# Kernel optimization log

Hardware: AMD Instinct MI355X
Metric: run time of the kernel (lower is better)

## Reference

```python
import jax, jax.numpy as jnp
import numpy as np

IN_F = 4096
OUT_F = 4096
RANK = 16
NUM_SLOTS = 32
ALPHA = 1.0


def setup_inputs() -> dict:
    key = jax.random.key(0)
    k_x, k_w, k_b, k_a, k_bm, k_idx = jax.random.split(key, 6)
    x = jax.random.normal(k_x, (8, 2048, IN_F), dtype=jnp.float32)
    weight = jax.random.normal(k_w, (OUT_F, IN_F), dtype=jnp.float32) * (1.0 / np.sqrt(IN_F))
    bias = jax.random.normal(k_b, (OUT_F,), dtype=jnp.float32) * 0.01
    lora_A = jax.random.normal(k_a, (NUM_SLOTS, IN_F, RANK), dtype=jnp.float32) * 1e-4
    lora_B = jax.random.normal(k_bm, (NUM_SLOTS, RANK, OUT_F), dtype=jnp.float32) * 1e-4
    lora_indices = jax.random.randint(k_idx, (8,), 0, NUM_SLOTS)
    return {"x": x, "weight": weight, "bias": bias, "lora_A": lora_A,
            "lora_B": lora_B, "lora_indices": lora_indices}


def reference(x, weight, bias, lora_A, lora_B, lora_indices):
    # base linear: x @ W.T + b
    out = jnp.einsum('bsd,od->bso', x, weight) + bias
    # per-sample LoRA slot gather + low-rank bmm chain
    chosen_A = lora_A[lora_indices]          # [B, in, r]
    chosen_B = lora_B[lora_indices]          # [B, r, out]
    inter = jnp.einsum('bsd,bdr->bsr', x, chosen_A)       # [B, S, r]
    out_lora = jnp.einsum('bsr,bro->bso', inter, chosen_B)  # [B, S, out]
    return out + ALPHA * out_lora
```

## Files before the change

### kernel.cpp

```cpp
#include <hip/hip_runtime.h>
#include <hip/hip_bf16.h>


#define M_TOT 16384
#define K_TOT 4096
#define N_TOT 4096
#define RANK 16
#define NT 128

typedef __attribute__((ext_vector_type(8))) short bf16x8;
typedef __attribute__((ext_vector_type(4))) float f32x4;

__device__ __forceinline__ unsigned short f2bf(float f) {
  unsigned int u = __builtin_bit_cast(unsigned int, f);
  u += 0x7fffu + ((u >> 16) & 1u);
  return (unsigned short)(u >> 16);
}

__global__ void cvt_bf16_kernel(const float* __restrict__ src,
                                unsigned short* __restrict__ dst, int n4) {
  int i = blockIdx.x * blockDim.x + threadIdx.x;
  const int stride = gridDim.x * blockDim.x;
  for (; i < n4; i += stride) {
    const float4 v = reinterpret_cast<const float4*>(src)[i];
    ushort4 o;
    o.x = f2bf(v.x); o.y = f2bf(v.y); o.z = f2bf(v.z); o.w = f2bf(v.w);
    reinterpret_cast<ushort4*>(dst)[i] = o;
  }
}

__global__ __launch_bounds__(256) void lora_inter_mfma_kernel(
    const unsigned short* __restrict__ xb,
    const float* __restrict__ loraA,
    const int* __restrict__ idx,
    float* __restrict__ inter) {
  const int lane = threadIdx.x & 63;
  const int wv = threadIdx.x >> 6;
  const int m0 = blockIdx.x * 64 + wv * 16;
  const int slot = idx[m0 >> 11];
  const int q = lane >> 4;
  const int c = lane & 15;
  const unsigned short* __restrict__ xrow = xb + (size_t)(m0 + c) * K_TOT + q * 8;
  const float* __restrict__ Abase = loraA + (size_t)slot * K_TOT * RANK + c;

  f32x4 acc = (f32x4){0.f, 0.f, 0.f, 0.f};
#pragma unroll 4
  for (int kt = 0; kt < K_TOT; kt += 32) {
    const bf16x8 af = *reinterpret_cast<const bf16x8*>(xrow + kt);
    const float* __restrict__ Ak = Abase + (size_t)(kt + q * 8) * RANK;
    bf16x8 bfr;
#pragma unroll
    for (int j = 0; j < 8; ++j) bfr[j] = (short)f2bf(Ak[(size_t)j * RANK]);
    acc = __builtin_amdgcn_mfma_f32_16x16x32_bf16(af, bfr, acc, 0, 0, 0);
  }
#pragma unroll
  for (int i = 0; i < 4; ++i)
    inter[(size_t)(m0 + q * 4 + i) * RANK + c] = acc[i];
}

__device__ __forceinline__ void gload16(const void* g, void* l) {
  __builtin_amdgcn_global_load_lds(
      (const __attribute__((address_space(1))) unsigned int*)g,
      (__attribute__((address_space(3))) unsigned int*)l, 16, 0, 0);
}

#define GBARRIER() asm volatile("s_barrier" ::: "memory")

__global__ __launch_bounds__(512, 2) void gemm_fused_kernel(
    const unsigned short* __restrict__ xb,
    const unsigned short* __restrict__ wb,
    const float* __restrict__ bias,
    const float* __restrict__ inter,
    const float* __restrict__ loraB,
    const int* __restrict__ idx,
    float* __restrict__ out) {
  __shared__ unsigned short lds[4][16384];
  char* ldsB = (char*)&lds[0][0];

  const int tid = threadIdx.x;
  const int lane = tid & 63;
  const int wv = tid >> 6;
  const int wr = wv >> 2;
  const int wc = wv & 3;

  const int bid = ((blockIdx.x & 7) << 7) | (blockIdx.x >> 3);
  const int m0 = (bid >> 4) << 8;
  const int n0 = (bid & 15) << 8;

  const int srow = tid >> 2;
  const int sslot = (tid & 3) ^ ((srow >> 1) & 3);
  const unsigned short* xs0 = xb + (size_t)(m0 + srow) * K_TOT + sslot * 8;
  const unsigned short* xs1 = xs0 + (size_t)128 * K_TOT;
  const unsigned short* ws0 = wb + (size_t)(n0 + srow) * K_TOT + sslot * 8;
  const unsigned short* ws1 = ws0 + (size_t)128 * K_TOT;
  const int stgoff = wv << 10;

#define STAGE_T(t)                                                  \
  do {                                                              \
    const int _bo = (((t) & 3) << 15);                              \
    gload16(xs0 + (size_t)(t) * 32, ldsB + _bo + stgoff);           \
    gload16(xs1 + (size_t)(t) * 32, ldsB + _bo + 8192 + stgoff);    \
    gload16(ws0 + (size_t)(t) * 32, ldsB + _bo + 16384 + stgoff);   \
    gload16(ws1 + (size_t)(t) * 32, ldsB + _bo + 24576 + stgoff);   \
  } while (0)

  const int rl = lane & 15;
  const int q = lane >> 4;
  const int pslot = ((q ^ ((rl >> 1) & 3)) << 4);
  const int aoff = (wr * 128 + rl) * 64 + pslot;
  const int boff = 16384 + (wc * 64 + rl) * 64 + pslot;

  f32x4 acc[8][4];
#pragma unroll
  for (int i = 0; i < 8; ++i)
#pragma unroll
    for (int j = 0; j < 4; ++j) acc[i][j] = (f32x4){0.f, 0.f, 0.f, 0.f};

  STAGE_T(0); STAGE_T(1); STAGE_T(2);
  asm volatile("s_waitcnt vmcnt(8)" ::: "memory");
  GBARRIER();

#pragma unroll 1
  for (int t = 0; t < NT; ++t) {
    const char* Ab = ldsB + ((t & 3) << 15) + aoff;
    const char* Bb = ldsB + ((t & 3) << 15) + boff;

    bf16x8 bfrag[4], afrag[8];
#pragma unroll
    for (int nf = 0; nf < 4; ++nf)
      bfrag[nf] = *reinterpret_cast<const bf16x8*>(Bb + nf * 1024);
#pragma unroll
    for (int mf = 0; mf < 8; ++mf)
      afrag[mf] = *reinterpret_cast<const bf16x8*>(Ab + mf * 1024);
    if (t < NT - 3) STAGE_T(t + 3);

    asm volatile("s_waitcnt lgkmcnt(0)" ::: "memory");
    __builtin_amdgcn_sched_barrier(0);
    __builtin_amdgcn_s_setprio(1);
#pragma unroll
    for (int mf = 0; mf < 8; ++mf)
#pragma unroll
      for (int nf = 0; nf < 4; ++nf)
        acc[mf][nf] = __builtin_amdgcn_mfma_f32_16x16x32_bf16(
            afrag[mf], bfrag[nf], acc[mf][nf], 0, 0, 0);
    __builtin_amdgcn_s_setprio(0);
    __builtin_amdgcn_sched_barrier(0);

    if (t < NT - 4) {
      asm volatile("s_waitcnt vmcnt(8)" ::: "memory");
    } else if (t == NT - 4) {
      asm volatile("s_waitcnt vmcnt(8)" ::: "memory");
    } else if (t == NT - 3) {
      asm volatile("s_waitcnt vmcnt(4)" ::: "memory");
    } else {
      asm volatile("s_waitcnt vmcnt(0)" ::: "memory");
    }
    GBARRIER();
  }

  const int slot = idx[m0 >> 11];
  const float* __restrict__ Bmat = loraB + (size_t)slot * RANK * N_TOT;
  const int gn0 = n0 + wc * 64 + rl;

  float bcv[4][RANK];
  float bv[4];
#pragma unroll
  for (int nf = 0; nf < 4; ++nf) {
    const int gn = gn0 + nf * 16;
    bv[nf] = bias[gn];
#pragma unroll
    for (int p = 0; p < RANK; ++p) bcv[nf][p] = Bmat[(size_t)p * N_TOT + gn];
  }
#pragma unroll
  for (int mf = 0; mf < 8; ++mf) {
    const int gmb = m0 + wr * 128 + mf * 16 + (q << 2);
#pragma unroll
    for (int r = 0; r < 4; ++r) {
      const int gm = gmb + r;
      const float4* ivp = reinterpret_cast<const float4*>(inter + (size_t)gm * RANK);
      const float4 iv0 = ivp[0], iv1 = ivp[1], iv2 = ivp[2], iv3 = ivp[3];
      float* orow = out + (size_t)gm * N_TOT;
#pragma unroll
      for (int nf = 0; nf < 4; ++nf) {
        const float lora =
            iv0.x * bcv[nf][0]  + iv0.y * bcv[nf][1]  + iv0.z * bcv[nf][2]  + iv0.w * bcv[nf][3] +
            iv1.x * bcv[nf][4]  + iv1.y * bcv[nf][5]  + iv1.z * bcv[nf][6]  + iv1.w * bcv[nf][7] +
            iv2.x * bcv[nf][8]  + iv2.y * bcv[nf][9]  + iv2.z * bcv[nf][10] + iv2.w * bcv[nf][11] +
            iv3.x * bcv[nf][12] + iv3.y * bcv[nf][13] + iv3.z * bcv[nf][14] + iv3.w * bcv[nf][15];
        orow[gn0 + nf * 16] = acc[mf][nf][r] + bv[nf] + lora;
      }
    }
  }
#undef STAGE_T
}

extern "C" void kernel_launch(void* const* d_in, const int* in_sizes, int n_in,
                              void* d_out, int out_size, void* d_ws, size_t ws_size,
                              hipStream_t stream) {
  const float* x     = (const float*)d_in[0];
  const float* w     = (const float*)d_in[1];
  const float* bias  = (const float*)d_in[2];
  const float* loraA = (const float*)d_in[3];
  const float* loraB = (const float*)d_in[4];
  const int*   idx   = (const int*)d_in[5];
  float* out = (float*)d_out;

  char* ws = (char*)d_ws;
  unsigned short* xb   = (unsigned short*)ws;
  unsigned short* wbuf = (unsigned short*)(ws + 134217728);
  float* inter = (float*)(ws + 134217728 + 33554432);

  cvt_bf16_kernel<<<2048, 256, 0, stream>>>(x, xb, M_TOT * K_TOT / 4);
  cvt_bf16_kernel<<<1024, 256, 0, stream>>>(w, wbuf, N_TOT * K_TOT / 4);
  lora_inter_mfma_kernel<<<M_TOT / 64, 256, 0, stream>>>(xb, loraA, idx, inter);
  gemm_fused_kernel<<<(M_TOT / 256) * (N_TOT / 256), 512, 0, stream>>>(
      xb, wbuf, bias, inter, loraB, idx, out);
}
```

Measured before the change: 671.8 us.

## Double-buffer LDS fragments in registers and interleave reads with MFMA groups

The GEMM main loop now keeps two register sets of A/B fragments. The fragments for the next K tile are read from LDS in chunks between four groups of MFMAs, with the global-to-LDS staging issued mid-tile, so LDS latency hides behind matrix math instead of stalling before each tile. The loop is unrolled by two to swap the fragment sets, and the vmcnt waits are tightened to match the new order of issued loads. This doubles fragment register usage, which may pressure the 2-blocks-per-CU occupancy target.

```diff
diff --git a/kernel.cpp b/kernel.cpp
--- a/kernel.cpp
+++ b/kernel.cpp
@@ -65,6 +65,7 @@
 }
 
 #define GBARRIER() asm volatile("s_barrier" ::: "memory")
+#define RD(p) (*reinterpret_cast<const bf16x8*>(p))
 
 __global__ __launch_bounds__(512, 2) void gemm_fused_kernel(
     const unsigned short* __restrict__ xb,
@@ -116,46 +117,88 @@
 #pragma unroll
     for (int j = 0; j < 4; ++j) acc[i][j] = (f32x4){0.f, 0.f, 0.f, 0.f};
 
+  bf16x8 fa[8], fb[4], ga[8], gb[4];
+#pragma unroll
+  for (int i = 0; i < 8; ++i) ga[i] = (bf16x8){0,0,0,0,0,0,0,0};
+#pragma unroll
+  for (int i = 0; i < 4; ++i) gb[i] = (bf16x8){0,0,0,0,0,0,0,0};
+
   STAGE_T(0); STAGE_T(1); STAGE_T(2);
-  asm volatile("s_waitcnt vmcnt(8)" ::: "memory");
+  asm volatile("s_waitcnt vmcnt(4)" ::: "memory");
   GBARRIER();
+  {
+    const char* Ab0 = ldsB + aoff;
+    const char* Bb0 = ldsB + boff;
+#pragma unroll
+    for (int i = 0; i < 8; ++i) fa[i] = RD(Ab0 + i * 1024);
+#pragma unroll
+    for (int i = 0; i < 4; ++i) fb[i] = RD(Bb0 + i * 1024);
+  }
+
+#define MG(CA, CB, g)                                                     \
+  do {                                                                    \
+    _Pragma("unroll")                                                     \
+    for (int nf = 0; nf < 4; ++nf)                                        \
+      acc[2 * (g)][nf] = __builtin_amdgcn_mfma_f32_16x16x32_bf16(         \
+          CA[2 * (g)], CB[nf], acc[2 * (g)][nf], 0, 0, 0);                \
+    _Pragma("unroll")                                                     \
+    for (int nf = 0; nf < 4; ++nf)                                        \
+      acc[2 * (g) + 1][nf] = __builtin_amdgcn_mfma_f32_16x16x32_bf16(     \
+          CA[2 * (g) + 1], CB[nf], acc[2 * (g) + 1][nf], 0, 0, 0);        \
+  } while (0)
+
+#define TILE_BODY(CA, CB, NA, NB, T)                                      \
+  do {                                                                    \
+    const int _t = (T);                                                   \
+    const char* Abn = ldsB + (((_t + 1) & 3) << 15) + aoff;               \
+    const char* Bbn = ldsB + (((_t + 1) & 3) << 15) + boff;               \
+    const bool rd = _t < NT - 1;                                          \
+    asm volatile("s_waitcnt lgkmcnt(0)" ::: "memory");                    \
+    __builtin_amdgcn_sched_barrier(0);                                    \
+    __builtin_amdgcn_s_setprio(1);                                        \
+    MG(CA, CB, 0);                                                        \
+    __builtin_amdgcn_s_setprio(0);                                        \
+    __builtin_amdgcn_sched_barrier(0);                                    \
+    if (rd) {                                                             \
+      NA[0] = RD(Abn);          NA[1] = RD(Abn + 1024);                   \
+      NA[2] = RD(Abn + 2048);   NA[3] = RD(Abn + 3072);                   \
+    }                                                                     \
+    __builtin_amdgcn_sched_barrier(0);                                    \
+    __builtin_amdgcn_s_setprio(1);                                        \
+    MG(CA, CB, 1);                                                        \
+    __builtin_amdgcn_s_setprio(0);                                        \
+    __builtin_amdgcn_sched_barrier(0);                                    \
+    if (rd) {                                                             \
+      NA[4] = RD(Abn + 4096);   NA[5] = RD(Abn + 5120);                   \
+      NA[6] = RD(Abn + 6144);   NA[7] = RD(Abn + 7168);                   \
+    }                                                                     \
+    __builtin_amdgcn_sched_barrier(0);                                    \
+    __builtin_amdgcn_s_setprio(1);                                        \
+    MG(CA, CB, 2);                                                        \
+    __builtin_amdgcn_s_setprio(0);                                        \
+    __builtin_amdgcn_sched_barrier(0);                                    \
+    if (rd) {                                                             \
+      NB[0] = RD(Bbn);          NB[1] = RD(Bbn + 1024);                   \
+      NB[2] = RD(Bbn + 2048);   NB[3] = RD(Bbn + 3072);                   \
+    }                                                                     \
+    if (_t < NT - 3) STAGE_T(_t + 3);                                     \
+    __builtin_amdgcn_sched_barrier(0);                                    \
+    __builtin_amdgcn_s_setprio(1);                                        \
+    MG(CA, CB, 3);                                                        \
+    __builtin_amdgcn_s_setprio(0);                                        \
+    __builtin_amdgcn_sched_barrier(0);                                    \
+    if (_t <= NT - 4) {                                                   \
+      asm volatile("s_waitcnt vmcnt(4)" ::: "memory");                    \
+    } else {                                                              \
+      asm volatile("s_waitcnt vmcnt(0)" ::: "memory");                    \
+    }                                                                     \
+    GBARRIER();                                                           \
+  } while (0)
 
 #pragma unroll 1
-  for (int t = 0; t < NT; ++t) {
-    const char* Ab = ldsB + ((t & 3) << 15) + aoff;
-    const char* Bb = ldsB + ((t & 3) << 15) + boff;
-
-    bf16x8 bfrag[4], afrag[8];
-#pragma unroll
-    for (int nf = 0; nf < 4; ++nf)
-      bfrag[nf] = *reinterpret_cast<const bf16x8*>(Bb + nf * 1024);
-#pragma unroll
-    for (int mf = 0; mf < 8; ++mf)
-      afrag[mf] = *reinterpret_cast<const bf16x8*>(Ab + mf * 1024);
-    if (t < NT - 3) STAGE_T(t + 3);
-
-    asm volatile("s_waitcnt lgkmcnt(0)" ::: "memory");
-    __builtin_amdgcn_sched_barrier(0);
-    __builtin_amdgcn_s_setprio(1);
-#pragma unroll
-    for (int mf = 0; mf < 8; ++mf)
-#pragma unroll
-      for (int nf = 0; nf < 4; ++nf)
-        acc[mf][nf] = __builtin_amdgcn_mfma_f32_16x16x32_bf16(
-            afrag[mf], bfrag[nf], acc[mf][nf], 0, 0, 0);
-    __builtin_amdgcn_s_setprio(0);
-    __builtin_amdgcn_sched_barrier(0);
-
-    if (t < NT - 4) {
-      asm volatile("s_waitcnt vmcnt(8)" ::: "memory");
-    } else if (t == NT - 4) {
-      asm volatile("s_waitcnt vmcnt(8)" ::: "memory");
-    } else if (t == NT - 3) {
-      asm volatile("s_waitcnt vmcnt(4)" ::: "memory");
-    } else {
-      asm volatile("s_waitcnt vmcnt(0)" ::: "memory");
-    }
-    GBARRIER();
+  for (int tp = 0; tp < NT; tp += 2) {
+    TILE_BODY(fa, fb, ga, gb, tp);
+    TILE_BODY(ga, gb, fa, fb, tp + 1);
   }
 
   const int slot = idx[m0 >> 11];
@@ -192,6 +235,8 @@
     }
   }
 #undef STAGE_T
+#undef TILE_BODY
+#undef MG
 }
 
 extern "C" void kernel_launch(void* const* d_in, const int* in_sizes, int n_in,
```

After: 664.0 us. About the same (-1.2%).

## Use 1024-thread GEMM blocks with smaller per-wave tiles and LDS-staged LoRA epilogue

Applied to the files above, without the earlier changes.

Doubles the GEMM block to 16 waves, each computing a 64x64 sub-tile instead of 128x64. Each thread now issues half as many global-to-LDS loads per stage, and the vmcnt waits are adjusted to match. The epilogue stages the inter rows, the LoRA B slice and the bias into LDS, then reads them from there instead of issuing scattered global loads. The aim is to cut register pressure and hide latency with more waves. The cost is less fragment reuse per wave and more LDS read traffic per MFMA. The 1024-thread launch bound also limits the registers available to each thread.

```diff
diff --git a/kernel.cpp b/kernel.cpp
--- a/kernel.cpp
+++ b/kernel.cpp
@@ -66,7 +66,7 @@
 
 #define GBARRIER() asm volatile("s_barrier" ::: "memory")
 
-__global__ __launch_bounds__(512, 2) void gemm_fused_kernel(
+__global__ __launch_bounds__(1024, 4) void gemm_fused_kernel(
     const unsigned short* __restrict__ xb,
     const unsigned short* __restrict__ wb,
     const float* __restrict__ bias,
@@ -89,35 +89,31 @@
 
   const int srow = tid >> 2;
   const int sslot = (tid & 3) ^ ((srow >> 1) & 3);
-  const unsigned short* xs0 = xb + (size_t)(m0 + srow) * K_TOT + sslot * 8;
-  const unsigned short* xs1 = xs0 + (size_t)128 * K_TOT;
-  const unsigned short* ws0 = wb + (size_t)(n0 + srow) * K_TOT + sslot * 8;
-  const unsigned short* ws1 = ws0 + (size_t)128 * K_TOT;
+  const unsigned short* xsrc = xb + (size_t)(m0 + srow) * K_TOT + sslot * 8;
+  const unsigned short* wsrc = wb + (size_t)(n0 + srow) * K_TOT + sslot * 8;
   const int stgoff = wv << 10;
 
 #define STAGE_T(t)                                                  \
   do {                                                              \
     const int _bo = (((t) & 3) << 15);                              \
-    gload16(xs0 + (size_t)(t) * 32, ldsB + _bo + stgoff);           \
-    gload16(xs1 + (size_t)(t) * 32, ldsB + _bo + 8192 + stgoff);    \
-    gload16(ws0 + (size_t)(t) * 32, ldsB + _bo + 16384 + stgoff);   \
-    gload16(ws1 + (size_t)(t) * 32, ldsB + _bo + 24576 + stgoff);   \
+    gload16(xsrc + (size_t)(t) * 32, ldsB + _bo + stgoff);          \
+    gload16(wsrc + (size_t)(t) * 32, ldsB + _bo + 16384 + stgoff);  \
   } while (0)
 
   const int rl = lane & 15;
   const int q = lane >> 4;
   const int pslot = ((q ^ ((rl >> 1) & 3)) << 4);
-  const int aoff = (wr * 128 + rl) * 64 + pslot;
+  const int aoff = (wr * 64 + rl) * 64 + pslot;
   const int boff = 16384 + (wc * 64 + rl) * 64 + pslot;
 
-  f32x4 acc[8][4];
-#pragma unroll
-  for (int i = 0; i < 8; ++i)
+  f32x4 acc[4][4];
+#pragma unroll
+  for (int i = 0; i < 4; ++i)
 #pragma unroll
     for (int j = 0; j < 4; ++j) acc[i][j] = (f32x4){0.f, 0.f, 0.f, 0.f};
 
   STAGE_T(0); STAGE_T(1); STAGE_T(2);
-  asm volatile("s_waitcnt vmcnt(8)" ::: "memory");
+  asm volatile("s_waitcnt vmcnt(4)" ::: "memory");
   GBARRIER();
 
 #pragma unroll 1
@@ -125,12 +121,12 @@
     const char* Ab = ldsB + ((t & 3) << 15) + aoff;
     const char* Bb = ldsB + ((t & 3) << 15) + boff;
 
-    bf16x8 bfrag[4], afrag[8];
+    bf16x8 afrag[4], bfrag[4];
 #pragma unroll
     for (int nf = 0; nf < 4; ++nf)
       bfrag[nf] = *reinterpret_cast<const bf16x8*>(Bb + nf * 1024);
 #pragma unroll
-    for (int mf = 0; mf < 8; ++mf)
+    for (int mf = 0; mf < 4; ++mf)
       afrag[mf] = *reinterpret_cast<const bf16x8*>(Ab + mf * 1024);
     if (t < NT - 3) STAGE_T(t + 3);
 
@@ -138,7 +134,7 @@
     __builtin_amdgcn_sched_barrier(0);
     __builtin_amdgcn_s_setprio(1);
 #pragma unroll
-    for (int mf = 0; mf < 8; ++mf)
+    for (int mf = 0; mf < 4; ++mf)
 #pragma unroll
       for (int nf = 0; nf < 4; ++nf)
         acc[mf][nf] = __builtin_amdgcn_mfma_f32_16x16x32_bf16(
@@ -146,12 +142,10 @@
     __builtin_amdgcn_s_setprio(0);
     __builtin_amdgcn_sched_barrier(0);
 
-    if (t < NT - 4) {
-      asm volatile("s_waitcnt vmcnt(8)" ::: "memory");
-    } else if (t == NT - 4) {
-      asm volatile("s_waitcnt vmcnt(8)" ::: "memory");
+    if (t <= NT - 4) {
+      asm volatile("s_waitcnt vmcnt(4)" ::: "memory");
     } else if (t == NT - 3) {
-      asm volatile("s_waitcnt vmcnt(4)" ::: "memory");
+      asm volatile("s_waitcnt vmcnt(2)" ::: "memory");
     } else {
       asm volatile("s_waitcnt vmcnt(0)" ::: "memory");
     }
@@ -160,36 +154,45 @@
 
   const int slot = idx[m0 >> 11];
   const float* __restrict__ Bmat = loraB + (size_t)slot * RANK * N_TOT;
-  const int gn0 = n0 + wc * 64 + rl;
-
-  float bcv[4][RANK];
-  float bv[4];
+  {
+    const int irow = tid >> 2, ipart = tid & 3;
+    gload16(inter + (size_t)(m0 + irow) * RANK + ipart * 4, ldsB + tid * 16);
+    const int p = tid >> 6, bpart = tid & 63;
+    gload16(Bmat + (size_t)p * N_TOT + n0 + bpart * 4,
+            ldsB + 16384 + p * 1024 + bpart * 16);
+    if (wv == 0) gload16(bias + n0 + lane * 4, ldsB + 32768 + lane * 16);
+  }
+  asm volatile("s_waitcnt vmcnt(0)" ::: "memory");
+  GBARRIER();
+
 #pragma unroll
   for (int nf = 0; nf < 4; ++nf) {
-    const int gn = gn0 + nf * 16;
-    bv[nf] = bias[gn];
-#pragma unroll
-    for (int p = 0; p < RANK; ++p) bcv[nf][p] = Bmat[(size_t)p * N_TOT + gn];
-  }
-#pragma unroll
-  for (int mf = 0; mf < 8; ++mf) {
-    const int gmb = m0 + wr * 128 + mf * 16 + (q << 2);
-#pragma unroll
-    for (int r = 0; r < 4; ++r) {
-      const int gm = gmb + r;
-      const float4* ivp = reinterpret_cast<const float4*>(inter + (size_t)gm * RANK);
-      const float4 iv0 = ivp[0], iv1 = ivp[1], iv2 = ivp[2], iv3 = ivp[3];
-      float* orow = out + (size_t)gm * N_TOT;
-#pragma unroll
-      for (int nf = 0; nf < 4; ++nf) {
+    const int col = wc * 64 + nf * 16 + rl;
+    const int gn = n0 + col;
+    const float bv = *reinterpret_cast<const float*>(ldsB + 32768 + col * 4);
+    float bcv[RANK];
+#pragma unroll
+    for (int p = 0; p < RANK; ++p)
+      bcv[p] = *reinterpret_cast<const float*>(ldsB + 16384 + p * 1024 + col * 4);
+#pragma unroll
+    for (int mf = 0; mf < 4; ++mf) {
+#pragma unroll
+      for (int r = 0; r < 4; ++r) {
+        const int row = wr * 64 + mf * 16 + (q << 2) + r;
+        const char* iRow = ldsB + row * 64;
+        const float4 iv0 = *reinterpret_cast<const float4*>(iRow);
+        const float4 iv1 = *reinterpret_cast<const float4*>(iRow + 16);
+        const float4 iv2 = *reinterpret_cast<const float4*>(iRow + 32);
+        const float4 iv3 = *reinterpret_cast<const float4*>(iRow + 48);
         const float lora =
-            iv0.x * bcv[nf][0]  + iv0.y * bcv[nf][1]  + iv0.z * bcv[nf][2]  + iv0.w * bcv[nf][3] +
-            iv1.x * bcv[nf][4]  + iv1.y * bcv[nf][5]  + iv1.z * bcv[nf][6]  + iv1.w * bcv[nf][7] +
-            iv2.x * bcv[nf][8]  + iv2.y * bcv[nf][9]  + iv2.z * bcv[nf][10] + iv2.w * bcv[nf][11] +
-            iv3.x * bcv[nf][12] + iv3.y * bcv[nf][13] + iv3.z * bcv[nf][14] + iv3.w * bcv[nf][15];
-        orow[gn0 + nf * 16] = acc[mf][nf][r] + bv[nf] + lora;
+            iv0.x * bcv[0]  + iv0.y * bcv[1]  + iv0.z * bcv[2]  + iv0.w * bcv[3] +
+            iv1.x * bcv[4]  + iv1.y * bcv[5]  + iv1.z * bcv[6]  + iv1.w * bcv[7] +
+            iv2.x * bcv[8]  + iv2.y * bcv[9]  + iv2.z * bcv[10] + iv2.w * bcv[11] +
+            iv3.x * bcv[12] + iv3.y * bcv[13] + iv3.z * bcv[14] + iv3.w * bcv[15];
+        out[(size_t)(m0 + row) * N_TOT + gn] = acc[mf][nf][r] + bv + lora;
       }
     }
+    asm volatile("" ::: "memory");
   }
 #undef STAGE_T
 }
@@ -213,6 +216,6 @@
   cvt_bf16_kernel<<<2048, 256, 0, stream>>>(x, xb, M_TOT * K_TOT / 4);
   cvt_bf16_kernel<<<1024, 256, 0, stream>>>(w, wbuf, N_TOT * K_TOT / 4);
   lora_inter_mfma_kernel<<<M_TOT / 64, 256, 0, stream>>>(xb, loraA, idx, inter);
-  gemm_fused_kernel<<<(M_TOT / 256) * (N_TOT / 256), 512, 0, stream>>>(
+  gemm_fused_kernel<<<(M_TOT / 256) * (N_TOT / 256), 1024, 0, stream>>>(
       xb, wbuf, bias, inter, loraB, idx, out);
 }
```

Result: slower. 718.2 us (+6.9%).

## Shrink GEMM tile to 256x128 with 4 waves and 3-buffer LDS ring

Applied to the files above, without the earlier changes.

The fused GEMM block tile changes from 256x256 with 8 waves to 256x128 with 4 waves of 256 threads. The LDS ring also drops from 4 stages to 3 stages of 24 KB each, with a prefetch distance of 2. The smaller LDS footprint lets two blocks share a CU and doubles the grid, aiming for better latency hiding and finer scheduling. In exchange each block reuses less data, so L2 and global traffic per FLOP rises, and the prefetch pipeline is shallower.

```diff
diff --git a/kernel.cpp b/kernel.cpp
--- a/kernel.cpp
+++ b/kernel.cpp
@@ -65,8 +65,9 @@
 }
 
 #define GBARRIER() asm volatile("s_barrier" ::: "memory")
-
-__global__ __launch_bounds__(512, 2) void gemm_fused_kernel(
+#define BUFSZ 24576
+
+__global__ __launch_bounds__(256, 2) void gemm_fused_kernel(
     const unsigned short* __restrict__ xb,
     const unsigned short* __restrict__ wb,
     const float* __restrict__ bias,
@@ -74,34 +75,34 @@
     const float* __restrict__ loraB,
     const int* __restrict__ idx,
     float* __restrict__ out) {
-  __shared__ unsigned short lds[4][16384];
-  char* ldsB = (char*)&lds[0][0];
+  __shared__ unsigned short lds[3 * BUFSZ / 2];
+  char* ldsB = (char*)lds;
 
   const int tid = threadIdx.x;
   const int lane = tid & 63;
   const int wv = tid >> 6;
-  const int wr = wv >> 2;
-  const int wc = wv & 3;
-
-  const int bid = ((blockIdx.x & 7) << 7) | (blockIdx.x >> 3);
-  const int m0 = (bid >> 4) << 8;
-  const int n0 = (bid & 15) << 8;
-
-  const int srow = tid >> 2;
-  const int sslot = (tid & 3) ^ ((srow >> 1) & 3);
-  const unsigned short* xs0 = xb + (size_t)(m0 + srow) * K_TOT + sslot * 8;
-  const unsigned short* xs1 = xs0 + (size_t)128 * K_TOT;
-  const unsigned short* ws0 = wb + (size_t)(n0 + srow) * K_TOT + sslot * 8;
-  const unsigned short* ws1 = ws0 + (size_t)128 * K_TOT;
-  const int stgoff = wv << 10;
-
-#define STAGE_T(t)                                                  \
-  do {                                                              \
-    const int _bo = (((t) & 3) << 15);                              \
-    gload16(xs0 + (size_t)(t) * 32, ldsB + _bo + stgoff);           \
-    gload16(xs1 + (size_t)(t) * 32, ldsB + _bo + 8192 + stgoff);    \
-    gload16(ws0 + (size_t)(t) * 32, ldsB + _bo + 16384 + stgoff);   \
-    gload16(ws1 + (size_t)(t) * 32, ldsB + _bo + 24576 + stgoff);   \
+  const int wr = wv >> 1;
+  const int wc = wv & 1;
+
+  const int bid = ((blockIdx.x & 7) << 8) | (blockIdx.x >> 3);
+  const int m0 = (bid >> 5) << 8;
+  const int n0 = (bid & 31) << 7;
+
+  const int r0 = tid >> 2;
+  const int scol = ((tid & 3) ^ ((r0 >> 1) & 3)) << 3;
+  const unsigned short* xsrc = xb + (size_t)(m0 + r0) * K_TOT + scol;
+  const unsigned short* wsrc = wb + (size_t)(n0 + r0) * K_TOT + scol;
+  const int stg = tid << 4;
+
+#define STAGE_T(t, bo)                                                   \
+  do {                                                                   \
+    const size_t _ko = (size_t)(t) * 32;                                 \
+    gload16(xsrc + _ko,                       ldsB + (bo) + stg);        \
+    gload16(xsrc + (size_t)64  * K_TOT + _ko, ldsB + (bo) + 4096 + stg); \
+    gload16(xsrc + (size_t)128 * K_TOT + _ko, ldsB + (bo) + 8192 + stg); \
+    gload16(xsrc + (size_t)192 * K_TOT + _ko, ldsB + (bo) + 12288 + stg);\
+    gload16(wsrc + _ko,                       ldsB + (bo) + 16384 + stg);\
+    gload16(wsrc + (size_t)64  * K_TOT + _ko, ldsB + (bo) + 20480 + stg);\
   } while (0)
 
   const int rl = lane & 15;
@@ -116,14 +117,17 @@
 #pragma unroll
     for (int j = 0; j < 4; ++j) acc[i][j] = (f32x4){0.f, 0.f, 0.f, 0.f};
 
-  STAGE_T(0); STAGE_T(1); STAGE_T(2);
-  asm volatile("s_waitcnt vmcnt(8)" ::: "memory");
+  STAGE_T(0, 0); STAGE_T(1, BUFSZ);
+  asm volatile("s_waitcnt vmcnt(6)" ::: "memory");
   GBARRIER();
+
+  int curoff = 0;
+  int stgoff3 = 2 * BUFSZ;
 
 #pragma unroll 1
   for (int t = 0; t < NT; ++t) {
-    const char* Ab = ldsB + ((t & 3) << 15) + aoff;
-    const char* Bb = ldsB + ((t & 3) << 15) + boff;
+    const char* Ab = ldsB + curoff + aoff;
+    const char* Bb = ldsB + curoff + boff;
 
     bf16x8 bfrag[4], afrag[8];
 #pragma unroll
@@ -132,7 +136,7 @@
 #pragma unroll
     for (int mf = 0; mf < 8; ++mf)
       afrag[mf] = *reinterpret_cast<const bf16x8*>(Ab + mf * 1024);
-    if (t < NT - 3) STAGE_T(t + 3);
+    if (t <= NT - 3) STAGE_T(t + 2, stgoff3);
 
     asm volatile("s_waitcnt lgkmcnt(0)" ::: "memory");
     __builtin_amdgcn_sched_barrier(0);
@@ -146,16 +150,15 @@
     __builtin_amdgcn_s_setprio(0);
     __builtin_amdgcn_sched_barrier(0);
 
-    if (t < NT - 4) {
-      asm volatile("s_waitcnt vmcnt(8)" ::: "memory");
-    } else if (t == NT - 4) {
-      asm volatile("s_waitcnt vmcnt(8)" ::: "memory");
-    } else if (t == NT - 3) {
-      asm volatile("s_waitcnt vmcnt(4)" ::: "memory");
+    if (t <= NT - 3) {
+      asm volatile("s_waitcnt vmcnt(6)" ::: "memory");
     } else {
       asm volatile("s_waitcnt vmcnt(0)" ::: "memory");
     }
     GBARRIER();
+
+    curoff = (curoff == 2 * BUFSZ) ? 0 : curoff + BUFSZ;
+    stgoff3 = (stgoff3 == 2 * BUFSZ) ? 0 : stgoff3 + BUFSZ;
   }
 
   const int slot = idx[m0 >> 11];
@@ -213,6 +216,6 @@
   cvt_bf16_kernel<<<2048, 256, 0, stream>>>(x, xb, M_TOT * K_TOT / 4);
   cvt_bf16_kernel<<<1024, 256, 0, stream>>>(w, wbuf, N_TOT * K_TOT / 4);
   lora_inter_mfma_kernel<<<M_TOT / 64, 256, 0, stream>>>(xb, loraA, idx, inter);
-  gemm_fused_kernel<<<(M_TOT / 256) * (N_TOT / 256), 512, 0, stream>>>(
+  gemm_fused_kernel<<<(M_TOT / 256) * (N_TOT / 128), 256, 0, stream>>>(
       xb, wbuf, bias, inter, loraB, idx, out);
 }
```

Result: slower. 706.0 us (+5.1%).
